# Kernel tuning notes

Hardware: AMD Instinct MI355X
Metric: run time of the kernel (lower is better)

## Reference

```python
import jax, jax.numpy as jnp
import numpy as np

N = 33554432  # number of flattened prediction/target points (~128 MB fp32 each)


def setup_inputs() -> dict:
    key = jax.random.key(0)
    k1, k2 = jax.random.split(key)
    predicted = jax.random.uniform(k1, (N,), dtype=jnp.float32)
    target = jax.random.uniform(k2, (N,), dtype=jnp.float32)
    weights = jnp.array([1.0, 2.0, 4.0, 8.0, 16.0], dtype=jnp.float32)
    edge = jnp.array([0.0, 0.1, 0.25, 0.5, 0.75, 1.0], dtype=jnp.float32)
    return {"predicted": predicted, "target": target, "weights": weights, "edge": edge}


def reference(predicted, target, weights, edge):
    # Original loops over bins: elements with edge[i] < t <= edge[i+1] get weight[i];
    # elements outside (edge[0], edge[-1]] are DROPPED (weight 0).
    nbins = weights.shape[0]
    # digitize(..., right=True): returns i s.t. edge[i-1] < t <= edge[i]; shift to bin index
    bin_idx = jnp.digitize(target, edge, right=True) - 1  # [N] int
    valid = (bin_idx >= 0) & (bin_idx < nbins)
    w = jnp.where(valid, weights[jnp.clip(bin_idx, 0, nbins - 1)], 0.0)
    loss = jnp.sum(w * (predicted - target) ** 2) / jnp.sum(weights)
    return loss
```

## Files before the change

kernel.cpp:

```cpp
#include <hip/hip_runtime.h>


__global__ void wmse_zero_kernel(float* out, int n) {
    int i = blockIdx.x * blockDim.x + threadIdx.x;
    if (i < n) out[i] = 0.0f;
}

__device__ __forceinline__ float wmse_elem(float p, float t,
                                           float e0, float e1, float e2,
                                           float e3, float e4, float e5,
                                           float w0, float w1, float w2,
                                           float w3, float w4) {
    float w = 0.0f;
    w = (t > e0 && t <= e1) ? w0 : w;
    w = (t > e1 && t <= e2) ? w1 : w;
    w = (t > e2 && t <= e3) ? w2 : w;
    w = (t > e3 && t <= e4) ? w3 : w;
    w = (t > e4 && t <= e5) ? w4 : w;
    float d = p - t;
    return w * d * d;
}

__global__ __launch_bounds__(256) void WeightedMSELoss_60335700574782_kernel(
    const float* __restrict__ pred, const float* __restrict__ targ,
    const float* __restrict__ weights, const float* __restrict__ edge,
    float* __restrict__ out, long long n) {
    const float e0 = edge[0], e1 = edge[1], e2 = edge[2];
    const float e3 = edge[3], e4 = edge[4], e5 = edge[5];
    const float w0 = weights[0], w1 = weights[1], w2 = weights[2];
    const float w3 = weights[3], w4 = weights[4];
    const float inv_wsum = 1.0f / (w0 + w1 + w2 + w3 + w4);

    const long long n4 = n >> 2;
    const long long tid = (long long)blockIdx.x * blockDim.x + threadIdx.x;
    const long long stride = (long long)gridDim.x * blockDim.x;

    const float4* __restrict__ p4 = (const float4*)pred;
    const float4* __restrict__ t4 = (const float4*)targ;

    float acc = 0.0f;
    for (long long i = tid; i < n4; i += stride) {
        float4 p = p4[i];
        float4 t = t4[i];
        acc += wmse_elem(p.x, t.x, e0, e1, e2, e3, e4, e5, w0, w1, w2, w3, w4);
        acc += wmse_elem(p.y, t.y, e0, e1, e2, e3, e4, e5, w0, w1, w2, w3, w4);
        acc += wmse_elem(p.z, t.z, e0, e1, e2, e3, e4, e5, w0, w1, w2, w3, w4);
        acc += wmse_elem(p.w, t.w, e0, e1, e2, e3, e4, e5, w0, w1, w2, w3, w4);
    }
    for (long long i = (n4 << 2) + tid; i < n; i += stride) {
        acc += wmse_elem(pred[i], targ[i], e0, e1, e2, e3, e4, e5, w0, w1, w2, w3, w4);
    }

    #pragma unroll
    for (int off = 32; off > 0; off >>= 1)
        acc += __shfl_down(acc, off, 64);

    __shared__ float smem[4];
    const int lane = threadIdx.x & 63;
    const int wid = threadIdx.x >> 6;
    if (lane == 0) smem[wid] = acc;
    __syncthreads();
    if (threadIdx.x == 0) {
        float bsum = smem[0] + smem[1] + smem[2] + smem[3];
        atomicAdd(out, bsum * inv_wsum);
    }
}

extern "C" void kernel_launch(void* const* d_in, const int* in_sizes, int n_in,
                              void* d_out, int out_size, void* d_ws, size_t ws_size,
                              hipStream_t stream) {
    const float* pred    = (const float*)d_in[0];
    const float* targ    = (const float*)d_in[1];
    const float* weights = (const float*)d_in[2];
    const float* edge    = (const float*)d_in[3];
    float* out = (float*)d_out;
    const long long n = (long long)in_sizes[0];

    wmse_zero_kernel<<<1, 64, 0, stream>>>(out, out_size);

    const int block = 256;
    long long n4 = n >> 2;
    int grid = (int)((n4 + block - 1) / block);
    if (grid > 2048) grid = 2048;
    if (grid < 1) grid = 1;
    WeightedMSELoss_60335700574782_kernel<<<grid, block, 0, stream>>>(
        pred, targ, weights, edge, out, n);
}
```

Baseline: 289.6 us.

## Use one-vector-per-thread grid with slotted partial sums and finish kernel

The grid-stride loop capped at 2048 blocks is replaced by a full grid of one float4 pair per thread, giving 32768 blocks. Block sums go by atomicAdd into 2048 workspace slots instead of a single output address, which spreads atomic contention. A new single-block finish kernel sums the slots, handles the scalar tail and applies the weight normalisation. The cost is a much larger number of blocks to launch, plus an extra kernel launch and a workspace zeroing pass.

```diff
diff --git a/kernel.cpp b/kernel.cpp
--- a/kernel.cpp
+++ b/kernel.cpp
@@ -1,9 +1,10 @@
 #include <hip/hip_runtime.h>
 
 
-__global__ void wmse_zero_kernel(float* out, int n) {
-    int i = blockIdx.x * blockDim.x + threadIdx.x;
-    if (i < n) out[i] = 0.0f;
+#define NSLOTS 2048
+
+__global__ void wmse_zero_ws(float* __restrict__ ws) {
+    ws[blockIdx.x * blockDim.x + threadIdx.x] = 0.0f;
 }
 
 __device__ __forceinline__ float wmse_elem(float p, float t,
@@ -23,32 +24,25 @@
 
 __global__ __launch_bounds__(256) void WeightedMSELoss_60335700574782_kernel(
     const float* __restrict__ pred, const float* __restrict__ targ,
-    const float* __restrict__ weights, const float* __restrict__ edge,
-    float* __restrict__ out, long long n) {
+    const float* __restrict__ edge, const float* __restrict__ weights,
+    float* __restrict__ partial, long long n4) {
     const float e0 = edge[0], e1 = edge[1], e2 = edge[2];
     const float e3 = edge[3], e4 = edge[4], e5 = edge[5];
     const float w0 = weights[0], w1 = weights[1], w2 = weights[2];
     const float w3 = weights[3], w4 = weights[4];
-    const float inv_wsum = 1.0f / (w0 + w1 + w2 + w3 + w4);
 
-    const long long n4 = n >> 2;
-    const long long tid = (long long)blockIdx.x * blockDim.x + threadIdx.x;
-    const long long stride = (long long)gridDim.x * blockDim.x;
-
+    const long long i = (long long)blockIdx.x * blockDim.x + threadIdx.x;
     const float4* __restrict__ p4 = (const float4*)pred;
     const float4* __restrict__ t4 = (const float4*)targ;
 
     float acc = 0.0f;
-    for (long long i = tid; i < n4; i += stride) {
+    if (i < n4) {
         float4 p = p4[i];
         float4 t = t4[i];
-        acc += wmse_elem(p.x, t.x, e0, e1, e2, e3, e4, e5, w0, w1, w2, w3, w4);
+        acc  = wmse_elem(p.x, t.x, e0, e1, e2, e3, e4, e5, w0, w1, w2, w3, w4);
         acc += wmse_elem(p.y, t.y, e0, e1, e2, e3, e4, e5, w0, w1, w2, w3, w4);
         acc += wmse_elem(p.z, t.z, e0, e1, e2, e3, e4, e5, w0, w1, w2, w3, w4);
         acc += wmse_elem(p.w, t.w, e0, e1, e2, e3, e4, e5, w0, w1, w2, w3, w4);
-    }
-    for (long long i = (n4 << 2) + tid; i < n; i += stride) {
-        acc += wmse_elem(pred[i], targ[i], e0, e1, e2, e3, e4, e5, w0, w1, w2, w3, w4);
     }
 
     #pragma unroll
@@ -62,8 +56,40 @@
     __syncthreads();
     if (threadIdx.x == 0) {
         float bsum = smem[0] + smem[1] + smem[2] + smem[3];
-        atomicAdd(out, bsum * inv_wsum);
+        atomicAdd(&partial[blockIdx.x & (NSLOTS - 1)], bsum);
     }
+}
+
+__global__ __launch_bounds__(256) void wmse_finish_kernel(
+    const float* __restrict__ partial,
+    const float* __restrict__ pred, const float* __restrict__ targ,
+    const float* __restrict__ edge, const float* __restrict__ weights,
+    float* __restrict__ out, long long n) {
+    const float e0 = edge[0], e1 = edge[1], e2 = edge[2];
+    const float e3 = edge[3], e4 = edge[4], e5 = edge[5];
+    const float w0 = weights[0], w1 = weights[1], w2 = weights[2];
+    const float w3 = weights[3], w4 = weights[4];
+    const float inv_wsum = 1.0f / (w0 + w1 + w2 + w3 + w4);
+
+    float acc = 0.0f;
+    for (int i = threadIdx.x; i < NSLOTS; i += blockDim.x)
+        acc += partial[i];
+
+    const long long n4 = n >> 2;
+    for (long long j = (n4 << 2) + threadIdx.x; j < n; j += blockDim.x)
+        acc += wmse_elem(pred[j], targ[j], e0, e1, e2, e3, e4, e5, w0, w1, w2, w3, w4);
+
+    #pragma unroll
+    for (int off = 32; off > 0; off >>= 1)
+        acc += __shfl_down(acc, off, 64);
+
+    __shared__ float smem[4];
+    const int lane = threadIdx.x & 63;
+    const int wid = threadIdx.x >> 6;
+    if (lane == 0) smem[wid] = acc;
+    __syncthreads();
+    if (threadIdx.x == 0)
+        out[0] = (smem[0] + smem[1] + smem[2] + smem[3]) * inv_wsum;
 }
 
 extern "C" void kernel_launch(void* const* d_in, const int* in_sizes, int n_in,
@@ -74,15 +100,17 @@
     const float* weights = (const float*)d_in[2];
     const float* edge    = (const float*)d_in[3];
     float* out = (float*)d_out;
+    float* partial = (float*)d_ws;
     const long long n = (long long)in_sizes[0];
+    const long long n4 = n >> 2;
 
-    wmse_zero_kernel<<<1, 64, 0, stream>>>(out, out_size);
+    wmse_zero_ws<<<NSLOTS / 256, 256, 0, stream>>>(partial);
 
     const int block = 256;
-    long long n4 = n >> 2;
-    int grid = (int)((n4 + block - 1) / block);
-    if (grid > 2048) grid = 2048;
-    if (grid < 1) grid = 1;
+    const int grid = (int)((n4 + block - 1) / block);
     WeightedMSELoss_60335700574782_kernel<<<grid, block, 0, stream>>>(
-        pred, targ, weights, edge, out, n);
+        pred, targ, edge, weights, partial, n4);
+
+    wmse_finish_kernel<<<1, block, 0, stream>>>(
+        partial, pred, targ, edge, weights, out, n);
 }
```

Measured after the change: 272.8 us. 5.8% less time.
